# Optimization experiments

Hardware: AMD Instinct MI355X
Metric: run time of the kernel (lower is better)

The kernel has to match this reference:

```python
import jax, jax.numpy as jnp
import numpy as np

VOCAB = 100000
DIM = 128
BATCH = 65536
N_NEG = 10


def setup_inputs() -> dict:
    key = jax.random.key(0)
    k1, k2, k3, k4, k5 = jax.random.split(key, 5)
    return {
        "pos_u": jax.random.randint(k1, (BATCH,), 0, VOCAB),
        "pos_v": jax.random.randint(k2, (BATCH,), 0, VOCAB),
        "neg_v": jax.random.randint(k3, (BATCH, N_NEG), 0, VOCAB),
        "u_weight": 0.01 * jax.random.normal(k4, (VOCAB, DIM), dtype=jnp.float32),
        "v_weight": 0.01 * jax.random.normal(k5, (VOCAB, DIM), dtype=jnp.float32),
    }


def reference(pos_u, pos_v, neg_v, u_weight, v_weight):
    emb_u = u_weight[pos_u]            # [B, D]
    emb_v = v_weight[pos_v]            # [B, D]
    emb_neg_v = v_weight[neg_v]        # [B, N, D]

    score = jnp.sum(emb_u * emb_v, axis=1)
    score = jnp.clip(score, -10.0, 10.0)
    score = -jax.nn.log_sigmoid(score)           # [B]

    neg_dots = jnp.einsum("bd,bnd->bn", emb_u, emb_neg_v)  # [B, N]
    # NOTE: faithful to source: neg term is ADDED (not negated) to the loss
    neg_score = jnp.sum(jax.nn.log_sigmoid(-neg_dots), axis=1)  # [B]

    return jnp.mean(score + neg_score)
```

## Files before the change

kernel.cpp:

```cpp
#include <hip/hip_runtime.h>

#define VOCAB 100000
#define DIM 128
#define BATCH 65536
#define N_NEG 10

#define BLOCKS (BATCH / 32)

__device__ __forceinline__ float dot4(float4 a, float4 b) {
    return a.x * b.x + a.y * b.y + a.z * b.z + a.w * b.w;
}

__device__ __forceinline__ float softplus_log2(float x) {
    const float y = x * 1.44269504f;
    const float t = __builtin_amdgcn_exp2f(-fabsf(y));
    return fmaxf(y, 0.0f) + __builtin_amdgcn_logf(1.0f + t);
}

__global__ void zero_out_kernel(float* out) { out[0] = 0.0f; }

__global__ __launch_bounds__(256) void skipgram_loss_kernel(
    const int* __restrict__ pos_u,
    const int* __restrict__ pos_v,
    const int* __restrict__ neg_v,
    const float4* __restrict__ u_weight,
    const float4* __restrict__ v_weight,
    float* __restrict__ out)
{
    const int tid  = threadIdx.x;
    const int lane = tid & 63;
    const int wave = tid >> 6;
    const int sub  = lane & 7;
    const int grp  = lane >> 3;

    const int b = (blockIdx.x * 4 + wave) * 8 + grp;

    const int iu = pos_u[b];
    const int iv = pos_v[b];

    const float4* __restrict__ urow = u_weight + iu * 32;
    float4 u0 = urow[0 * 8 + sub];
    float4 u1 = urow[1 * 8 + sub];
    float4 u2 = urow[2 * 8 + sub];
    float4 u3 = urow[3 * 8 + sub];

    const float4* __restrict__ vrow = v_weight + iv * 32;
    float p = dot4(u0, vrow[0 * 8 + sub]) + dot4(u1, vrow[1 * 8 + sub])
            + dot4(u2, vrow[2 * 8 + sub]) + dot4(u3, vrow[3 * 8 + sub]);

    float nd[N_NEG];
    #pragma unroll
    for (int n = 0; n < N_NEG; ++n) {
        const int idx = neg_v[b * N_NEG + n];
        const float4* __restrict__ wrow = v_weight + idx * 32;
        nd[n] = dot4(u0, wrow[0 * 8 + sub]) + dot4(u1, wrow[1 * 8 + sub])
              + dot4(u2, wrow[2 * 8 + sub]) + dot4(u3, wrow[3 * 8 + sub]);
    }

    #pragma unroll
    for (int m = 1; m < 8; m <<= 1) {
        p += __shfl_xor(p, m, 64);
        #pragma unroll
        for (int n = 0; n < N_NEG; ++n) nd[n] += __shfl_xor(nd[n], m, 64);
    }

    float s = fminf(fmaxf(p, -10.0f), 10.0f);
    float loss2 = softplus_log2(-s);
    #pragma unroll
    for (int n = 0; n < N_NEG; ++n)
        loss2 -= softplus_log2(nd[n]);
    float loss = loss2 * 0.69314718f;

    #pragma unroll
    for (int m = 8; m < 64; m <<= 1) loss += __shfl_xor(loss, m, 64);

    __shared__ float smem[4];
    if (lane == 0) smem[wave] = loss;
    __syncthreads();
    if (tid == 0) {
        atomicAdd(out, (smem[0] + smem[1] + smem[2] + smem[3]) * (1.0f / (float)BATCH));
    }
}

extern "C" void kernel_launch(void* const* d_in, const int* in_sizes, int n_in,
                              void* d_out, int out_size, void* d_ws, size_t ws_size,
                              hipStream_t stream) {
    const int*    pos_u    = (const int*)d_in[0];
    const int*    pos_v    = (const int*)d_in[1];
    const int*    neg_v    = (const int*)d_in[2];
    const float4* u_weight = (const float4*)d_in[3];
    const float4* v_weight = (const float4*)d_in[4];
    float* out = (float*)d_out;

    zero_out_kernel<<<1, 1, 0, stream>>>(out);
    skipgram_loss_kernel<<<BLOCKS, 256, 0, stream>>>(
        pos_u, pos_v, neg_v, u_weight, v_weight, out);
}
```

Before: 160.3 us.

## Quantize embedding tables to scaled fp8 in workspace before gathering dot products

Adds a pre-pass on every call that converts both fp32 embedding tables to fp8 e4m3, scaled by 256, into the workspace. The loss kernel then gathers 16-byte fp8 row slices instead of 64-byte fp32 slices and dequantizes them in registers. The aim is to cut the bytes moved by the random row gathers, which dominate the cost. In exchange it adds a full streaming read and write of both tables each call, and it loses precision in the dot products. The old fp32 kernel is kept as a fallback when the workspace is too small.

```diff
diff --git a/kernel.cpp b/kernel.cpp
--- a/kernel.cpp
+++ b/kernel.cpp
@@ -1,4 +1,5 @@
 #include <hip/hip_runtime.h>
+#include <hip/hip_fp8.h>
 
 #define VOCAB 100000
 #define DIM 128
@@ -6,9 +7,33 @@
 #define N_NEG 10
 
 #define BLOCKS (BATCH / 32)
-
-__device__ __forceinline__ float dot4(float4 a, float4 b) {
-    return a.x * b.x + a.y * b.y + a.z * b.z + a.w * b.w;
+#define QSCALE 256.0f
+#define QINV   (1.0f / (256.0f * 256.0f))
+
+__device__ __forceinline__ unsigned int pack4_fp8(float a, float b, float c, float d) {
+    unsigned int r =  (unsigned int)__hip_fp8_e4m3(a).__x;
+    r |= (unsigned int)__hip_fp8_e4m3(b).__x << 8;
+    r |= (unsigned int)__hip_fp8_e4m3(c).__x << 16;
+    r |= (unsigned int)__hip_fp8_e4m3(d).__x << 24;
+    return r;
+}
+
+__device__ __forceinline__ float fp8_to_f(unsigned int b) {
+    __hip_fp8_e4m3 t; t.__x = (__hip_fp8_storage_t)b; return (float)t;
+}
+
+__device__ __forceinline__ float dot16_fp8(uint4 w, const float* uf) {
+    float s = 0.0f;
+    const unsigned int ws[4] = {w.x, w.y, w.z, w.w};
+    #pragma unroll
+    for (int q = 0; q < 4; ++q) {
+        const unsigned int x = ws[q];
+        s += uf[q * 4 + 0] * fp8_to_f(x & 0xffu);
+        s += uf[q * 4 + 1] * fp8_to_f((x >> 8) & 0xffu);
+        s += uf[q * 4 + 2] * fp8_to_f((x >> 16) & 0xffu);
+        s += uf[q * 4 + 3] * fp8_to_f(x >> 24);
+    }
+    return s;
 }
 
 __device__ __forceinline__ float softplus_log2(float x) {
@@ -19,7 +44,89 @@
 
 __global__ void zero_out_kernel(float* out) { out[0] = 0.0f; }
 
-__global__ __launch_bounds__(256) void skipgram_loss_kernel(
+__global__ __launch_bounds__(256) void quantize_kernel(
+    const float4* __restrict__ in, uint4* __restrict__ out) {
+    const int i = blockIdx.x * 256 + threadIdx.x;
+    const float4 a = in[i * 4 + 0];
+    const float4 b = in[i * 4 + 1];
+    const float4 c = in[i * 4 + 2];
+    const float4 d = in[i * 4 + 3];
+    uint4 r;
+    r.x = pack4_fp8(a.x * QSCALE, a.y * QSCALE, a.z * QSCALE, a.w * QSCALE);
+    r.y = pack4_fp8(b.x * QSCALE, b.y * QSCALE, b.z * QSCALE, b.w * QSCALE);
+    r.z = pack4_fp8(c.x * QSCALE, c.y * QSCALE, c.z * QSCALE, c.w * QSCALE);
+    r.w = pack4_fp8(d.x * QSCALE, d.y * QSCALE, d.z * QSCALE, d.w * QSCALE);
+    out[i] = r;
+}
+
+__global__ __launch_bounds__(256) void skipgram_loss_fp8_kernel(
+    const int* __restrict__ pos_u,
+    const int* __restrict__ pos_v,
+    const int* __restrict__ neg_v,
+    const uint4* __restrict__ u8,
+    const uint4* __restrict__ v8,
+    float* __restrict__ out)
+{
+    const int tid  = threadIdx.x;
+    const int lane = tid & 63;
+    const int wave = tid >> 6;
+    const int sub  = lane & 7;
+    const int grp  = lane >> 3;
+
+    const int b = (blockIdx.x * 4 + wave) * 8 + grp;
+
+    const int iu = pos_u[b];
+    const int iv = pos_v[b];
+
+    const uint4 uq = u8[iu * 8 + sub];
+    float uf[16];
+    {
+        const unsigned int ws_[4] = {uq.x, uq.y, uq.z, uq.w};
+        #pragma unroll
+        for (int q = 0; q < 4; ++q) {
+            uf[q * 4 + 0] = fp8_to_f(ws_[q] & 0xffu);
+            uf[q * 4 + 1] = fp8_to_f((ws_[q] >> 8) & 0xffu);
+            uf[q * 4 + 2] = fp8_to_f((ws_[q] >> 16) & 0xffu);
+            uf[q * 4 + 3] = fp8_to_f(ws_[q] >> 24);
+        }
+    }
+
+    float acc[N_NEG + 1];
+    acc[0] = dot16_fp8(v8[iv * 8 + sub], uf);
+    #pragma unroll
+    for (int n = 0; n < N_NEG; ++n) {
+        const int idx = neg_v[b * N_NEG + n];
+        acc[n + 1] = dot16_fp8(v8[idx * 8 + sub], uf);
+    }
+
+    #pragma unroll
+    for (int m = 1; m < 8; m <<= 1) {
+        #pragma unroll
+        for (int j = 0; j <= N_NEG; ++j) acc[j] += __shfl_xor(acc[j], m, 64);
+    }
+
+    float s = fminf(fmaxf(acc[0] * QINV, -10.0f), 10.0f);
+    float loss2 = softplus_log2(-s);
+    #pragma unroll
+    for (int n = 0; n < N_NEG; ++n)
+        loss2 -= softplus_log2(acc[n + 1] * QINV);
+    float loss = loss2 * 0.69314718f;
+
+    #pragma unroll
+    for (int m = 8; m < 64; m <<= 1) loss += __shfl_xor(loss, m, 64);
+
+    __shared__ float smem[4];
+    if (lane == 0) smem[wave] = loss;
+    __syncthreads();
+    if (tid == 0)
+        atomicAdd(out, (smem[0] + smem[1] + smem[2] + smem[3]) * (1.0f / (float)BATCH));
+}
+
+__device__ __forceinline__ float dot4(float4 a, float4 b) {
+    return a.x * b.x + a.y * b.y + a.z * b.z + a.w * b.w;
+}
+
+__global__ __launch_bounds__(256) void skipgram_loss_fp32_kernel(
     const int* __restrict__ pos_u,
     const int* __restrict__ pos_v,
     const int* __restrict__ neg_v,
@@ -67,8 +174,7 @@
     float s = fminf(fmaxf(p, -10.0f), 10.0f);
     float loss2 = softplus_log2(-s);
     #pragma unroll
-    for (int n = 0; n < N_NEG; ++n)
-        loss2 -= softplus_log2(nd[n]);
+    for (int n = 0; n < N_NEG; ++n) loss2 -= softplus_log2(nd[n]);
     float loss = loss2 * 0.69314718f;
 
     #pragma unroll
@@ -77,9 +183,8 @@
     __shared__ float smem[4];
     if (lane == 0) smem[wave] = loss;
     __syncthreads();
-    if (tid == 0) {
+    if (tid == 0)
         atomicAdd(out, (smem[0] + smem[1] + smem[2] + smem[3]) * (1.0f / (float)BATCH));
-    }
 }
 
 extern "C" void kernel_launch(void* const* d_in, const int* in_sizes, int n_in,
@@ -93,6 +198,18 @@
     float* out = (float*)d_out;
 
     zero_out_kernel<<<1, 1, 0, stream>>>(out);
-    skipgram_loss_kernel<<<BLOCKS, 256, 0, stream>>>(
-        pos_u, pos_v, neg_v, u_weight, v_weight, out);
-}
+
+    const size_t table_bytes = (size_t)VOCAB * DIM;
+    if (ws_size >= 2 * table_bytes) {
+        uint4* u8 = (uint4*)d_ws;
+        uint4* v8 = (uint4*)((char*)d_ws + table_bytes);
+        const int qblocks = (VOCAB * DIM / 16) / 256;
+        quantize_kernel<<<qblocks, 256, 0, stream>>>(u_weight, u8);
+        quantize_kernel<<<qblocks, 256, 0, stream>>>(v_weight, v8);
+        skipgram_loss_fp8_kernel<<<BLOCKS, 256, 0, stream>>>(
+            pos_u, pos_v, neg_v, u8, v8, out);
+    } else {
+        skipgram_loss_fp32_kernel<<<BLOCKS, 256, 0, stream>>>(
+            pos_u, pos_v, neg_v, u_weight, v_weight, out);
+    }
+}
```

Result: slower. 170.3 us (+6.3%).
